# Kernel tuning notes

Hardware: AMD Instinct MI355X
Metric: run time of the kernel (lower is better)

## Reference

```python
import jax, jax.numpy as jnp
import numpy as np

B, N, M, DQ, DK, DV, H = 8, 1024, 1024, 512, 512, 512, 8
DH = DV // H           # per-head dim (dim_split)
DFF = 4 * DV           # FFN hidden dim
EPS = 1e-5


def _layernorm(x, g, b):
    mu = jnp.mean(x, axis=-1, keepdims=True)
    var = jnp.mean(jnp.square(x - mu), axis=-1, keepdims=True)
    return (x - mu) * jax.lax.rsqrt(var + EPS) * g + b


def setup_inputs() -> dict:
    key = jax.random.key(0)
    ks = jax.random.split(key, 20)
    s = 0.02
    return {
        "Q": jax.random.normal(ks[0], (B, N, DQ), jnp.float32),
        "K": jax.random.normal(ks[1], (B, M, DK), jnp.float32),
        "Wq": jax.random.normal(ks[2], (DV, DQ), jnp.float32) * s,
        "bq": jnp.zeros((DV,), jnp.float32),
        "Wk": jax.random.normal(ks[3], (DV, DK), jnp.float32) * s,
        "bk": jnp.zeros((DV,), jnp.float32),
        "Wv": jax.random.normal(ks[4], (DV, DK), jnp.float32) * s,
        "bv": jnp.zeros((DV,), jnp.float32),
        "W1": jax.random.normal(ks[5], (DFF, DV), jnp.float32) * s,
        "b1": jnp.zeros((DFF,), jnp.float32),
        "W2": jax.random.normal(ks[6], (DFF, DFF), jnp.float32) * s,
        "b2": jnp.zeros((DFF,), jnp.float32),
        "W3": jax.random.normal(ks[7], (DV, DFF), jnp.float32) * s,
        "b3": jnp.zeros((DV,), jnp.float32),
        "g0": jnp.ones((DV,), jnp.float32),
        "beta0": jnp.zeros((DV,), jnp.float32),
        "g1": jnp.ones((DV,), jnp.float32),
        "beta1": jnp.zeros((DV,), jnp.float32),
    }


def reference(Q, K, Wq, bq, Wk, bk, Wv, bv, W1, b1, W2, b2, W3, b3, g0, beta0, g1, beta1):
    # projections (torch Linear: x @ W.T + b)
    Qp = Q @ Wq.T + bq            # [B, N, DV]
    Kp = K @ Wk.T + bk            # [B, M, DV]
    Vp = K @ Wv.T + bv            # [B, M, DV]

    # split heads: [B, S, DV] -> [B, S, H, DH]
    Qh = Qp.reshape(B, N, H, DH)
    Kh = Kp.reshape(B, M, H, DH)
    Vh = Vp.reshape(B, M, H, DH)

    # scaled dot-product attention (scale = sqrt(head_dim))
    A = jnp.einsum("bnhd,bmhd->bhnm", Qh, Kh) / jnp.sqrt(jnp.float32(DH))
    A = jax.nn.softmax(A, axis=-1)
    O = jnp.einsum("bhnm,bmhd->bnhd", A, Vh).reshape(B, N, DV)

    # residual with projected Q, then LN
    O = _layernorm(O + Qp, g0, beta0)

    # FFN: Linear->ReLU->Linear->ReLU->Linear (num_hidden_layers=2)
    h = jax.nn.relu(O @ W1.T + b1)
    h = jax.nn.relu(h @ W2.T + b2)
    Off = h @ W3.T + b3

    return _layernorm(O + Off, g1, beta1)
```

## Files before the change

kernel.cpp:

```cpp
#include <hip/hip_runtime.h>


typedef __bf16 bf16_t;
typedef __bf16 bf16x8 __attribute__((ext_vector_type(8)));
typedef __bf16 bf16x4 __attribute__((ext_vector_type(4)));
typedef __bf16 bf16x2 __attribute__((ext_vector_type(2)));
typedef float  f32x4  __attribute__((ext_vector_type(4)));
typedef float  f32x16 __attribute__((ext_vector_type(16)));
typedef int    i32x4_t __attribute__((ext_vector_type(4)));
typedef int    i32x8_t __attribute__((ext_vector_type(8)));

__device__ __forceinline__ f32x4 mfma16(bf16x8 a, bf16x8 b, f32x4 c) {
  return __builtin_amdgcn_mfma_f32_16x16x32_bf16(a, b, c, 0, 0, 0);
}

__device__ __forceinline__ void gload_lds16(const void* g, void* l) {
  __builtin_amdgcn_global_load_lds((const __attribute__((address_space(1))) void*)g,
                                   (__attribute__((address_space(3))) void*)l,
                                   16, 0, 0);
}

__device__ __forceinline__ unsigned char to_fp8(float v) {
  return (unsigned char)(__builtin_amdgcn_cvt_pk_fp8_f32(v, v, 0, false) & 0xff);
}

__global__ __launch_bounds__(256) void cast_all(
    const float* __restrict__ Q, const float* __restrict__ K,
    const float* __restrict__ Wq, const float* __restrict__ Wk,
    const float* __restrict__ Wv, const float* __restrict__ W1,
    const float* __restrict__ W2, const float* __restrict__ W3,
    bf16_t* Qb, bf16_t* Kb, bf16_t* Wqb, bf16_t* Wkb, bf16_t* Wvb,
    bf16_t* W1b, unsigned char* W2q, bf16_t* W3b)
{
  long i = ((long)blockIdx.x * 256 + threadIdx.x) * 4;
  if (i >= 10223616L && i < 14417920L) {
    long o = i - 10223616L;
    float4 v = *(const float4*)(W2 + o);
    unsigned int lo = __builtin_amdgcn_cvt_pk_fp8_f32(v.x, v.y, 0, false);
    unsigned int hi = __builtin_amdgcn_cvt_pk_fp8_f32(v.z, v.w, 0, false);
    *(unsigned int*)(W2q + o) = (lo & 0xffffu) | (hi << 16);
    return;
  }
  const float* s; bf16_t* d; long o;
  if      (i <  4194304L) { s = Q;  d = Qb;  o = i;             }
  else if (i <  8388608L) { s = K;  d = Kb;  o = i - 4194304L;  }
  else if (i <  8650752L) { s = Wq; d = Wqb; o = i - 8388608L;  }
  else if (i <  8912896L) { s = Wk; d = Wkb; o = i - 8650752L;  }
  else if (i <  9175040L) { s = Wv; d = Wvb; o = i - 8912896L;  }
  else if (i < 10223616L) { s = W1; d = W1b; o = i - 9175040L;  }
  else                    { s = W3; d = W3b; o = i - 14417920L; }
  float4 v = *(const float4*)(s + o);
  bf16x4 w;
  w[0] = (bf16_t)v.x; w[1] = (bf16_t)v.y; w[2] = (bf16_t)v.z; w[3] = (bf16_t)v.w;
  *(bf16x4*)(d + o) = w;
}

template <int BM, bool RELU, bool VTEPI>
__device__ __forceinline__ void gemm_core(
    const bf16_t* __restrict__ A, const bf16_t* __restrict__ W,
    const float* __restrict__ bias, float* __restrict__ Cf,
    bf16_t* __restrict__ Cb, unsigned char* __restrict__ C8,
    bf16_t* __restrict__ VTout,
    float bscale, int N, int K, int lda, int ldb, int bx, int by)
{
  static_assert(BM == 128, "gemm_core tuned for BM=128");
  constexpr int FI = 4;
  constexpr int FJ = 4;
  constexpr int CN = 64;
  constexpr int AISS = 4;
  constexpr int SM_HALF = (BM + 128) * 64 * 2;
  constexpr int SMEM = 2 * SM_HALF;

  __shared__ __align__(16) char smem[SMEM];

  const int tid  = threadIdx.x;
  const int wave = tid >> 6, lane = tid & 63;
  const int lq   = lane & 15, quad = lane >> 4;
  const int wm   = wave & 1;
  const int wn   = wave >> 1;
  const long row0 = (long)bx * BM;
  const long col0 = (long)by * 128;

  const int sr = tid >> 3;
  const int cg = (tid & 7) ^ (sr & 7);
  const bf16_t* ag = A + (row0 + sr) * (long)lda + cg * 8;
  const bf16_t* bg = W + (col0 + sr) * (long)ldb + cg * 8;
  const int asOff = wave * 1024;
  const int bsOff = BM * 128 + wave * 1024;
  const long arows32 = 32L * lda;
  const long brows32 = 32L * ldb;

  auto stage = [&](int k0, int bi) {
    char* base = smem + bi * SM_HALF;
#pragma unroll
    for (int is = 0; is < AISS; is++)
      gload_lds16(ag + is * arows32 + k0, base + asOff + is * 4096);
#pragma unroll
    for (int is = 0; is < 4; is++)
      gload_lds16(bg + is * brows32 + k0, base + bsOff + is * 4096);
  };

  const int off0 = (quad ^ (lq & 7)) * 8;
  const int aO0 = ((wm * 64 + lq) * 64 + off0) * 2;
  const int aO1 = ((wm * 64 + lq) * 64 + (off0 ^ 32)) * 2;
  const int bO0 = BM * 128 + ((wn * CN + lq) * 64 + off0) * 2;
  const int bO1 = BM * 128 + ((wn * CN + lq) * 64 + (off0 ^ 32)) * 2;

  f32x4 acc[FI][FJ];
#pragma unroll
  for (int i = 0; i < FI; i++)
#pragma unroll
    for (int j = 0; j < FJ; j++) acc[i][j] = (f32x4){0.f, 0.f, 0.f, 0.f};

  stage(0, 0);
  const int nt = K >> 6;
  for (int t = 0; t < nt; ++t) {
    const int cur = t & 1;
    if (t < nt - 1) {
      stage((t + 1) * 64, cur ^ 1);
      asm volatile("s_waitcnt vmcnt(8)" ::: "memory");
    } else {
      asm volatile("s_waitcnt vmcnt(0)" ::: "memory");
    }
    __builtin_amdgcn_s_barrier();
    __builtin_amdgcn_sched_barrier(0);

    const char* base = smem + cur * SM_HALF;
    bf16x8 af[FI], bw[FJ];
#pragma unroll
    for (int i = 0; i < FI; i++) af[i] = *(const bf16x8*)(base + aO0 + i * 2048);
#pragma unroll
    for (int j = 0; j < FJ; j++) bw[j] = *(const bf16x8*)(base + bO0 + j * 2048);
#pragma unroll
    for (int i = 0; i < FI; i++)
#pragma unroll
      for (int j = 0; j < FJ; j++)
        acc[i][j] = mfma16(af[i], bw[j], acc[i][j]);
#pragma unroll
    for (int i = 0; i < FI; i++) af[i] = *(const bf16x8*)(base + aO1 + i * 2048);
#pragma unroll
    for (int j = 0; j < FJ; j++) bw[j] = *(const bf16x8*)(base + bO1 + j * 2048);
#pragma unroll
    for (int i = 0; i < FI; i++)
#pragma unroll
      for (int j = 0; j < FJ; j++)
        acc[i][j] = mfma16(af[i], bw[j], acc[i][j]);

    __builtin_amdgcn_sched_barrier(0);
    __builtin_amdgcn_s_barrier();
  }

  float bc[FJ];
#pragma unroll
  for (int j = 0; j < FJ; j++)
    bc[j] = bias ? bias[col0 + wn * CN + j * 16 + lq] : 0.f;

  if (VTEPI && VTout) {
    bf16_t* Ts = (bf16_t*)smem;
    __syncthreads();
#pragma unroll
    for (int i = 0; i < FI; i++)
#pragma unroll
      for (int j = 0; j < FJ; j++) {
        bf16x4 pv;
#pragma unroll
        for (int r = 0; r < 4; r++) pv[r] = (bf16_t)(acc[i][j][r] + bc[j]);
        *(bf16x4*)(Ts + (wn * CN + j * 16 + lq) * 132 + wm * 64 + i * 16 + quad * 4) = pv;
      }
    __syncthreads();
    const int b  = bx >> 3;
    const int mb = (bx & 7) * 128;
    const int h0 = by * 2;
    const int dd = tid >> 4;
    const int mc = (tid & 15) * 8;
#pragma unroll
    for (int p = 0; p < 8; p++) {
      const int d = dd + p * 16;
      bf16x8 v = *(const bf16x8*)(Ts + d * 132 + mc);
      *(bf16x8*)(VTout + ((long)(b * 8 + h0 + (d >> 6))) * 65536
                 + (d & 63) * 1024 + mb + mc) = v;
    }
    return;
  }

  const long rb = row0 + wm * 64 + quad * 4;
  const long cb = col0 + wn * CN + lq;
#pragma unroll
  for (int i = 0; i < FI; i++)
#pragma unroll
    for (int j = 0; j < FJ; j++)
#pragma unroll
      for (int r = 0; r < 4; r++) {
        float v = acc[i][j][r] + bc[j];
        if (RELU) v = fmaxf(v, 0.f);
        long idx = (rb + i * 16 + r) * (long)N + cb + j * 16;
        if (Cf) Cf[idx] = v;
        if (Cb) Cb[idx] = (bf16_t)(v * bscale);
        if (C8) C8[idx] = to_fp8(v);
      }
}

template <int BM, bool RELU>
__global__ __launch_bounds__(256) void gemm_bt(
    const bf16_t* __restrict__ A, const bf16_t* __restrict__ W,
    const float* __restrict__ bias, float* __restrict__ Cf,
    bf16_t* __restrict__ Cb, unsigned char* __restrict__ C8,
    float bscale, int N, int K)
{
  const int d  = blockIdx.x;
  const int bx = (d & 7) * 8 + ((d >> 3) & 7);
  const int by = d >> 6;
  gemm_core<BM, RELU, false>(A, W, bias, Cf, Cb, C8, nullptr, bscale,
                             N, K, K, K, bx, by);
}

__global__ __launch_bounds__(256) void ffn3_splitk(
    const bf16_t* __restrict__ H2, const bf16_t* __restrict__ W3b,
    bf16_t* __restrict__ Off01)
{
  const int z = blockIdx.z;
  gemm_core<128, false, false>(H2 + z * 1024, W3b + z * 1024, nullptr,
                               nullptr, Off01 + (long)z * 4194304, nullptr,
                               nullptr, 1.0f, 512, 1024, 2048, 2048,
                               blockIdx.x, blockIdx.y);
}

__global__ __launch_bounds__(256) void proj3(
    const bf16_t* __restrict__ Qb, const bf16_t* __restrict__ Kb,
    const bf16_t* __restrict__ Wqb, const bf16_t* __restrict__ Wkb,
    const bf16_t* __restrict__ Wvb,
    const float* __restrict__ bq, const float* __restrict__ bk,
    const float* __restrict__ bv,
    bf16_t* Qpb, bf16_t* Kpb, bf16_t* VT)
{
  const int z = blockIdx.z;
  const bf16_t* A  = (z == 0) ? Qb : Kb;
  const bf16_t* Wt = (z == 0) ? Wqb : ((z == 1) ? Wkb : Wvb);
  const float* bias = (z == 0) ? bq : ((z == 1) ? bk : bv);
  bf16_t* Cb = (z == 0) ? Qpb : ((z == 1) ? Kpb : nullptr);
  bf16_t* VTout = (z == 2) ? VT : nullptr;
  const float sc = (z == 1) ? 0.125f : 1.0f;
  gemm_core<128, false, true>(A, Wt, bias, nullptr, Cb, nullptr, VTout, sc,
                              512, 512, 512, 512, blockIdx.x, blockIdx.y);
}

__global__ __launch_bounds__(256) void ffn2_fp8(
    const unsigned char* __restrict__ H1, const unsigned char* __restrict__ W2,
    const float* __restrict__ bias, bf16_t* __restrict__ C)
{
  __shared__ unsigned char As[2][16384];
  __shared__ unsigned char Bs[2][16384];
  const int tid = threadIdx.x;
  const int wave = tid >> 6, lane = tid & 63;
  const int wm = wave & 1, wn = wave >> 1;
  const int m = lane & 31, h = lane >> 5;
  const int d  = blockIdx.x;
  const int bxi = (d & 7) * 8 + ((d >> 3) & 7);
  const int byi = d >> 6;
  const long row0 = (long)bxi * 128;
  const long col0 = (long)byi * 128;

  const int sr = tid >> 3;
  const int cg = (tid & 7) ^ (sr & 7);
  const unsigned char* ag = H1 + (row0 + sr) * 2048 + cg * 16;
  const unsigned char* bg = W2 + (col0 + sr) * 2048 + cg * 16;

  auto stage = [&](int k0, int bi) {
    char* asD = (char*)As[bi] + wave * 1024;
    char* bsD = (char*)Bs[bi] + wave * 1024;
#pragma unroll
    for (int is = 0; is < 4; is++)
      gload_lds16(ag + is * 65536 + k0, asD + is * 4096);
#pragma unroll
    for (int is = 0; is < 4; is++)
      gload_lds16(bg + is * 65536 + k0, bsD + is * 4096);
  };

  const int ar0 = wm * 64 + m, ar1 = ar0 + 32;
  const int br0 = wn * 64 + m, br1 = wn * 64 + 32 + m;

  f32x16 acc[2][2];
#pragma unroll
  for (int mi = 0; mi < 2; mi++)
#pragma unroll
    for (int nj = 0; nj < 2; nj++)
#pragma unroll
      for (int r = 0; r < 16; r++) acc[mi][nj][r] = 0.f;

  stage(0, 0);
  for (int t = 0; t < 16; ++t) {
    const int cur = t & 1;
    if (t < 15) {
      stage((t + 1) * 128, cur ^ 1);
      asm volatile("s_waitcnt vmcnt(8)" ::: "memory");
    } else {
      asm volatile("s_waitcnt vmcnt(0)" ::: "memory");
    }
    __builtin_amdgcn_s_barrier();
    __builtin_amdgcn_sched_barrier(0);

    const unsigned char* Ac = As[cur];
    const unsigned char* Bc = Bs[cur];
#pragma unroll
    for (int ks = 0; ks < 2; ks++) {
      const int c0 = ks * 4 + h * 2;
      i32x8_t a[2], b[2];
#pragma unroll
      for (int mi = 0; mi < 2; mi++) {
        const int r = mi ? ar1 : ar0;
        i32x4_t lo = *(const i32x4_t*)(Ac + r * 128 + ((c0    ) ^ (r & 7)) * 16);
        i32x4_t hi = *(const i32x4_t*)(Ac + r * 128 + ((c0 + 1) ^ (r & 7)) * 16);
        a[mi][0] = lo[0]; a[mi][1] = lo[1]; a[mi][2] = lo[2]; a[mi][3] = lo[3];
        a[mi][4] = hi[0]; a[mi][5] = hi[1]; a[mi][6] = hi[2]; a[mi][7] = hi[3];
      }
#pragma unroll
      for (int nj = 0; nj < 2; nj++) {
        const int r = nj ? br1 : br0;
        i32x4_t lo = *(const i32x4_t*)(Bc + r * 128 + ((c0    ) ^ (r & 7)) * 16);
        i32x4_t hi = *(const i32x4_t*)(Bc + r * 128 + ((c0 + 1) ^ (r & 7)) * 16);
        b[nj][0] = lo[0]; b[nj][1] = lo[1]; b[nj][2] = lo[2]; b[nj][3] = lo[3];
        b[nj][4] = hi[0]; b[nj][5] = hi[1]; b[nj][6] = hi[2]; b[nj][7] = hi[3];
      }
#pragma unroll
      for (int mi = 0; mi < 2; mi++)
#pragma unroll
        for (int nj = 0; nj < 2; nj++)
          acc[mi][nj] = __builtin_amdgcn_mfma_scale_f32_32x32x64_f8f6f4(
              a[mi], b[nj], acc[mi][nj], 0, 0,
              0, 0x7f7f7f7f, 0, 0x7f7f7f7f);
    }

    __builtin_amdgcn_sched_barrier(0);
    __builtin_amdgcn_s_barrier();
  }

  float bc[2];
  bc[0] = bias[col0 + wn * 64 + m];
  bc[1] = bias[col0 + wn * 64 + 32 + m];
#pragma unroll
  for (int mi = 0; mi < 2; mi++)
#pragma unroll
    for (int nj = 0; nj < 2; nj++)
#pragma unroll
      for (int reg = 0; reg < 16; reg++) {
        const int rl = (reg & 3) + 8 * (reg >> 2) + 4 * h;
        float v = fmaxf(acc[mi][nj][reg] + bc[nj], 0.f);
        C[(row0 + wm * 64 + mi * 32 + rl) * 2048 + col0 + wn * 64 + nj * 32 + m]
            = (bf16_t)v;
      }
}

__global__ __launch_bounds__(256) void attn(
    const bf16_t* __restrict__ Qp, const bf16_t* __restrict__ Kp,
    const bf16_t* __restrict__ VT, bf16_t* __restrict__ O)
{
  const int d0 = blockIdx.x;
  const int j  = d0 >> 3;
  const int g  = (d0 & 7) * 8 + (j >> 3);
  const int qb = j & 7;
  const int h  = g & 7, b = g >> 3;

  const int tid = threadIdx.x;
  const int wave = tid >> 6, lane = tid & 63;
  const int lq = lane & 15, quad = lane >> 4;

  __shared__ bf16_t Ks[2][8192];
  __shared__ bf16_t VTs[2][8192];
  __shared__ bf16_t Ps[4][16 * 72];

  const long bh = (long)b * 1024;
  const int qrowA = qb * 128 + wave * 16 + lq;
  const int qrowB = qrowA + 64;

  const bf16_t* qpA = Qp + (bh + qrowA) * 512 + h * 64 + quad * 8;
  const bf16_t* qpB = Qp + (bh + qrowB) * 512 + h * 64 + quad * 8;
  const bf16x8 qfA0 = *(const bf16x8*)qpA;
  const bf16x8 qfA1 = *(const bf16x8*)(qpA + 32);
  const bf16x8 qfB0 = *(const bf16x8*)qpB;
  const bf16x8 qfB1 = *(const bf16x8*)(qpB + 32);

  f32x4 oaccA[4], oaccB[4];
#pragma unroll
  for (int t = 0; t < 4; t++) {
    oaccA[t] = (f32x4){0.f, 0.f, 0.f, 0.f};
    oaccB[t] = (f32x4){0.f, 0.f, 0.f, 0.f};
  }
  float lA = 0.f, lB = 0.f;

  const int sr = tid >> 3;
  const int cg = (tid & 7) ^ (sr & 7);
  const bf16_t* kg  = Kp + bh * 512 + h * 64;
  const bf16_t* vtg = VT + ((long)b * 8 + h) * 65536;
  const int off0 = (quad ^ (lq & 7)) * 8;

  auto stage = [&](int m0, int bi) {
    char* ksDst = (char*)(Ks[bi]) + wave * 1024;
    char* vtDst = (char*)(VTs[bi]) + wave * 1024;
#pragma unroll
    for (int s = 0; s < 2; s++) {
      gload_lds16(kg + (long)(m0 + s * 64 + sr) * 512 + cg * 8,      ksDst + s * 8192);
      gload_lds16(kg + (long)(m0 + s * 64 + sr + 32) * 512 + cg * 8, ksDst + s * 8192 + 4096);
      gload_lds16(vtg + (long)sr * 1024 + m0 + s * 64 + cg * 8,        vtDst + s * 8192);
      gload_lds16(vtg + (long)(sr + 32) * 1024 + m0 + s * 64 + cg * 8, vtDst + s * 8192 + 4096);
    }
  };

  stage(0, 0);

  for (int t = 0; t < 8; ++t) {
    const int cur = t & 1;
    if (t < 7) {
      stage((t + 1) * 128, cur ^ 1);
      asm volatile("s_waitcnt vmcnt(8)" ::: "memory");
    } else {
      asm volatile("s_waitcnt vmcnt(0)" ::: "memory");
    }
    __builtin_amdgcn_s_barrier();
    __builtin_amdgcn_sched_barrier(0);

    const bf16_t* Kc = Ks[cur];
    const bf16_t* Vc = VTs[cur];

    f32x4 stA[8], stB[8];
#pragma unroll
    for (int tt = 0; tt < 8; tt++) {
      const bf16_t* kb = Kc + (tt >> 2) * 4096 + ((tt & 3) * 16 + lq) * 64;
      bf16x8 ka0 = *(const bf16x8*)(kb + off0);
      bf16x8 ka1 = *(const bf16x8*)(kb + (off0 ^ 32));
      f32x4 sA = (f32x4){0.f, 0.f, 0.f, 0.f};
      sA = mfma16(ka0, qfA0, sA);
      sA = mfma16(ka1, qfA1, sA);
      stA[tt] = sA;
      f32x4 sB = (f32x4){0.f, 0.f, 0.f, 0.f};
      sB = mfma16(ka0, qfB0, sB);
      sB = mfma16(ka1, qfB1, sB);
      stB[tt] = sB;
    }

    float lsA = 0.f, lsB = 0.f;
#pragma unroll
    for (int tt = 0; tt < 8; tt++)
#pragma unroll
      for (int r = 0; r < 4; r++) {
        float pA = __expf(stA[tt][r]);
        stA[tt][r] = pA;
        lsA += pA;
        float pB = __expf(stB[tt][r]);
        stB[tt][r] = pB;
        lsB += pB;
      }
    lsA += __shfl_xor(lsA, 16, 64);
    lsA += __shfl_xor(lsA, 32, 64);
    lA += lsA;
    lsB += __shfl_xor(lsB, 16, 64);
    lsB += __shfl_xor(lsB, 32, 64);
    lB += lsB;

    bf16_t* pw = &Ps[wave][0];
#pragma unroll
    for (int hh = 0; hh < 2; hh++) {
#pragma unroll
      for (int tt = 0; tt < 4; tt++) {
        bf16x4 pv;
#pragma unroll
        for (int r = 0; r < 4; r++) pv[r] = (bf16_t)stA[hh * 4 + tt][r];
        *(bf16x4*)(pw + lq * 72 + tt * 16 + quad * 4) = pv;
      }
#pragma unroll
      for (int ks = 0; ks < 2; ks++) {
        bf16x8 pb = *(const bf16x8*)(pw + lq * 72 + ks * 32 + quad * 8);
#pragma unroll
        for (int dt = 0; dt < 4; dt++) {
          const bf16_t* vb = Vc + hh * 4096 + (dt * 16 + lq) * 64;
          bf16x8 va = *(const bf16x8*)(vb + (ks ? (off0 ^ 32) : off0));
          oaccA[dt] = mfma16(va, pb, oaccA[dt]);
        }
      }
    }
#pragma unroll
    for (int hh = 0; hh < 2; hh++) {
#pragma unroll
      for (int tt = 0; tt < 4; tt++) {
        bf16x4 pv;
#pragma unroll
        for (int r = 0; r < 4; r++) pv[r] = (bf16_t)stB[hh * 4 + tt][r];
        *(bf16x4*)(pw + lq * 72 + tt * 16 + quad * 4) = pv;
      }
#pragma unroll
      for (int ks = 0; ks < 2; ks++) {
        bf16x8 pb = *(const bf16x8*)(pw + lq * 72 + ks * 32 + quad * 8);
#pragma unroll
        for (int dt = 0; dt < 4; dt++) {
          const bf16_t* vb = Vc + hh * 4096 + (dt * 16 + lq) * 64;
          bf16x8 va = *(const bf16x8*)(vb + (ks ? (off0 ^ 32) : off0));
          oaccB[dt] = mfma16(va, pb, oaccB[dt]);
        }
      }
    }

    __builtin_amdgcn_sched_barrier(0);
    __builtin_amdgcn_s_barrier();
  }

  const float invA = 1.f / lA;
  const float invB = 1.f / lB;
  bf16_t* opA = O + (bh + qrowA) * 512 + h * 64 + quad * 4;
  bf16_t* opB = O + (bh + qrowB) * 512 + h * 64 + quad * 4;
#pragma unroll
  for (int dt = 0; dt < 4; dt++) {
    bf16x4 vA, vB;
#pragma unroll
    for (int r = 0; r < 4; r++) {
      vA[r] = (bf16_t)(oaccA[dt][r] * invA);
      vB[r] = (bf16_t)(oaccB[dt][r] * invB);
    }
    *(bf16x4*)(opA + dt * 16) = vA;
    *(bf16x4*)(opB + dt * 16) = vB;
  }
}

__device__ __forceinline__ float2 ld2(const float* p, long row, int tid) {
  return ((const float2*)(p + row * 512))[tid];
}
__device__ __forceinline__ float2 ld2(const bf16_t* p, long row, int tid) {
  bf16x2 v = *(const bf16x2*)(p + row * 512 + tid * 2);
  return make_float2((float)v[0], (float)v[1]);
}

__device__ __forceinline__ void ln_finish(
    float x0, float x1, const float* g, const float* be, int tid,
    int wave, int lane, float* of, bf16_t* ob, long row)
{
  float s = x0 + x1, ss = x0 * x0 + x1 * x1;
#pragma unroll
  for (int off = 1; off < 64; off <<= 1) {
    s  += __shfl_xor(s,  off, 64);
    ss += __shfl_xor(ss, off, 64);
  }
  __shared__ float sm[8];
  if (lane == 0) { sm[wave] = s; sm[4 + wave] = ss; }
  __syncthreads();
  s  = sm[0] + sm[1] + sm[2] + sm[3];
  ss = sm[4] + sm[5] + sm[6] + sm[7];
  const float mu = s * (1.f / 512.f);
  const float var = ss * (1.f / 512.f) - mu * mu;
  const float rs = rsqrtf(var + 1e-5f);
  const float2 gg = ((const float2*)g)[tid];
  const float2 bb = ((const float2*)be)[tid];
  const float o0 = (x0 - mu) * rs * gg.x + bb.x;
  const float o1 = (x1 - mu) * rs * gg.y + bb.y;
  if (of) ((float2*)(of + row * 512))[tid] = make_float2(o0, o1);
  if (ob) {
    bf16x2 t; t[0] = (bf16_t)o0; t[1] = (bf16_t)o1;
    *(bf16x2*)(ob + row * 512 + tid * 2) = t;
  }
}

__global__ __launch_bounds__(256) void ln_res(
    const bf16_t* __restrict__ A, const bf16_t* __restrict__ Bv,
    const float* __restrict__ g, const float* __restrict__ be,
    bf16_t* __restrict__ ob)
{
  const int row = blockIdx.x, tid = threadIdx.x;
  const float2 va = ld2(A,  (long)row, tid);
  const float2 vb = ld2(Bv, (long)row, tid);
  ln_finish(va.x + vb.x, va.y + vb.y, g, be, tid, tid >> 6, tid & 63,
            nullptr, ob, row);
}

__global__ __launch_bounds__(256) void ln_res3(
    const bf16_t* __restrict__ X, const bf16_t* __restrict__ O0,
    const bf16_t* __restrict__ O1, const float* __restrict__ bias,
    const float* __restrict__ g, const float* __restrict__ be,
    float* __restrict__ of)
{
  const int row = blockIdx.x, tid = threadIdx.x;
  const float2 vx = ld2(X,  (long)row, tid);
  const float2 v0 = ld2(O0, (long)row, tid);
  const float2 v1 = ld2(O1, (long)row, tid);
  const float2 vb = ((const float2*)bias)[tid];
  ln_finish(vx.x + v0.x + v1.x + vb.x, vx.y + v0.y + v1.y + vb.y,
            g, be, tid, tid >> 6, tid & 63, of, nullptr, row);
}

extern "C" void kernel_launch(void* const* d_in, const int* in_sizes, int n_in,
                              void* d_out, int out_size, void* d_ws, size_t ws_size,
                              hipStream_t stream)
{
  const float* Q   = (const float*)d_in[0];
  const float* K   = (const float*)d_in[1];
  const float* Wq  = (const float*)d_in[2];
  const float* bq  = (const float*)d_in[3];
  const float* Wk  = (const float*)d_in[4];
  const float* bk  = (const float*)d_in[5];
  const float* Wv  = (const float*)d_in[6];
  const float* bv  = (const float*)d_in[7];
  const float* W1  = (const float*)d_in[8];
  const float* b1  = (const float*)d_in[9];
  const float* W2  = (const float*)d_in[10];
  const float* b2  = (const float*)d_in[11];
  const float* W3  = (const float*)d_in[12];
  const float* b3  = (const float*)d_in[13];
  const float* g0  = (const float*)d_in[14];
  const float* be0 = (const float*)d_in[15];
  const float* g1  = (const float*)d_in[16];
  const float* be1 = (const float*)d_in[17];

  char* ws = (char*)d_ws;
  bf16_t* Wqb = (bf16_t*)(ws + 0);
  bf16_t* Wkb = (bf16_t*)(ws + 524288);
  bf16_t* Wvb = (bf16_t*)(ws + 1048576);
  bf16_t* W1b = (bf16_t*)(ws + 1572864);
  bf16_t* W3b = (bf16_t*)(ws + 3670016);
  unsigned char* W2q = (unsigned char*)(ws + 5767168);
  bf16_t* Qb  = (bf16_t*)(ws + 14155776);
  bf16_t* Kb  = (bf16_t*)(ws + 22544384);
  bf16_t* Qpb = (bf16_t*)(ws + 30932992);
  bf16_t* Kpb = (bf16_t*)(ws + 39321600);
  bf16_t* VT  = (bf16_t*)(ws + 47710208);
  bf16_t* Of  = (bf16_t*)(ws + 14155776);
  bf16_t* Xb  = (bf16_t*)(ws + 22544384);
  bf16_t* H2  = (bf16_t*)(ws + 30932992);
  unsigned char* H1q = (unsigned char*)(ws + 64487424);
  bf16_t* Off0 = (bf16_t*)(ws + 64487424);
  bf16_t* Off1 = (bf16_t*)(ws + 72876032);
  float*  out = (float*)d_out;

  cast_all<<<15104, 256, 0, stream>>>(Q, K, Wq, Wk, Wv, W1, W2, W3,
                                      Qb, Kb, Wqb, Wkb, Wvb, W1b, W2q, W3b);
  proj3<<<dim3(64, 4, 3), 256, 0, stream>>>(Qb, Kb, Wqb, Wkb, Wvb, bq, bk, bv,
                                            Qpb, Kpb, VT);
  attn<<<dim3(512, 1, 1), 256, 0, stream>>>(Qpb, Kpb, VT, Of);
  ln_res<<<8192, 256, 0, stream>>>(Of, Qpb, g0, be0, Xb);
  gemm_bt<128, true ><<<dim3(1024, 1, 1), 256, 0, stream>>>(Xb, W1b, b1, nullptr, nullptr, H1q, 1.0f, 2048, 512);
  ffn2_fp8<<<dim3(1024, 1, 1), 256, 0, stream>>>(H1q, W2q, b2, H2);
  ffn3_splitk<<<dim3(64, 4, 2), 256, 0, stream>>>(H2, W3b, Off0);
  ln_res3<<<8192, 256, 0, stream>>>(Xb, Off0, Off1, b3, g1, be1, out);
}
```

Before: 271.4 us.

## Drop double buffering in ffn2, ffn3 and projection GEMMs to halve LDS

Adds a DBUF template flag to the shared GEMM core. The projection and FFN3 split-K kernels now use one LDS buffer with a sync, load, sync sequence per K tile, and the FP8 FFN2 kernel gets the same single-buffer loop. Halving shared memory per block should let more blocks fit on each CU, hiding latency through occupancy rather than in-block prefetch. The cost is that loads no longer overlap MFMA work inside a block, and each tile needs two full barriers.

```diff
diff --git a/kernel.cpp b/kernel.cpp
--- a/kernel.cpp
+++ b/kernel.cpp
@@ -55,7 +55,7 @@
   *(bf16x4*)(d + o) = w;
 }
 
-template <int BM, bool RELU, bool VTEPI>
+template <int BM, bool RELU, bool VTEPI, bool DBUF>
 __device__ __forceinline__ void gemm_core(
     const bf16_t* __restrict__ A, const bf16_t* __restrict__ W,
     const float* __restrict__ bias, float* __restrict__ Cf,
@@ -68,8 +68,10 @@
   constexpr int FJ = 4;
   constexpr int CN = 64;
   constexpr int AISS = 4;
-  constexpr int SM_HALF = (BM + 128) * 64 * 2;
-  constexpr int SMEM = 2 * SM_HALF;
+  constexpr int SM_AB = (BM + 128) * 64 * 2;
+  constexpr int SM_TS = 128 * 132 * 2;
+  constexpr int SM_ONE = (VTEPI && SM_TS > SM_AB) ? SM_TS : SM_AB;
+  constexpr int SMEM = DBUF ? 2 * SM_AB : SM_ONE;
 
   __shared__ __align__(16) char smem[SMEM];
 
@@ -91,7 +93,7 @@
   const long brows32 = 32L * ldb;
 
   auto stage = [&](int k0, int bi) {
-    char* base = smem + bi * SM_HALF;
+    char* base = smem + (DBUF ? bi * SM_AB : 0);
 #pragma unroll
     for (int is = 0; is < AISS; is++)
       gload_lds16(ag + is * arows32 + k0, base + asOff + is * 4096);
@@ -112,20 +114,28 @@
 #pragma unroll
     for (int j = 0; j < FJ; j++) acc[i][j] = (f32x4){0.f, 0.f, 0.f, 0.f};
 
-  stage(0, 0);
   const int nt = K >> 6;
+  if constexpr (DBUF) stage(0, 0);
   for (int t = 0; t < nt; ++t) {
-    const int cur = t & 1;
-    if (t < nt - 1) {
-      stage((t + 1) * 64, cur ^ 1);
-      asm volatile("s_waitcnt vmcnt(8)" ::: "memory");
+    const char* base;
+    if constexpr (DBUF) {
+      const int cur = t & 1;
+      if (t < nt - 1) {
+        stage((t + 1) * 64, cur ^ 1);
+        asm volatile("s_waitcnt vmcnt(8)" ::: "memory");
+      } else {
+        asm volatile("s_waitcnt vmcnt(0)" ::: "memory");
+      }
+      __builtin_amdgcn_s_barrier();
+      __builtin_amdgcn_sched_barrier(0);
+      base = smem + cur * SM_AB;
     } else {
-      asm volatile("s_waitcnt vmcnt(0)" ::: "memory");
-    }
-    __builtin_amdgcn_s_barrier();
-    __builtin_amdgcn_sched_barrier(0);
-
-    const char* base = smem + cur * SM_HALF;
+      __syncthreads();
+      stage(t * 64, 0);
+      __syncthreads();
+      base = smem;
+    }
+
     bf16x8 af[FI], bw[FJ];
 #pragma unroll
     for (int i = 0; i < FI; i++) af[i] = *(const bf16x8*)(base + aO0 + i * 2048);
@@ -146,8 +156,10 @@
       for (int j = 0; j < FJ; j++)
         acc[i][j] = mfma16(af[i], bw[j], acc[i][j]);
 
-    __builtin_amdgcn_sched_barrier(0);
-    __builtin_amdgcn_s_barrier();
+    if constexpr (DBUF) {
+      __builtin_amdgcn_sched_barrier(0);
+      __builtin_amdgcn_s_barrier();
+    }
   }
 
   float bc[FJ];
@@ -210,8 +222,8 @@
   const int d  = blockIdx.x;
   const int bx = (d & 7) * 8 + ((d >> 3) & 7);
   const int by = d >> 6;
-  gemm_core<BM, RELU, false>(A, W, bias, Cf, Cb, C8, nullptr, bscale,
-                             N, K, K, K, bx, by);
+  gemm_core<BM, RELU, false, true>(A, W, bias, Cf, Cb, C8, nullptr, bscale,
+                                   N, K, K, K, bx, by);
 }
 
 __global__ __launch_bounds__(256) void ffn3_splitk(
@@ -219,7 +231,7 @@
     bf16_t* __restrict__ Off01)
 {
   const int z = blockIdx.z;
-  gemm_core<128, false, false>(H2 + z * 1024, W3b + z * 1024, nullptr,
+  gemm_core<128, false, false, false>(H2 + z * 1024, W3b + z * 1024, nullptr,
                                nullptr, Off01 + (long)z * 4194304, nullptr,
                                nullptr, 1.0f, 512, 1024, 2048, 2048,
                                blockIdx.x, blockIdx.y);
@@ -240,7 +252,7 @@
   bf16_t* Cb = (z == 0) ? Qpb : ((z == 1) ? Kpb : nullptr);
   bf16_t* VTout = (z == 2) ? VT : nullptr;
   const float sc = (z == 1) ? 0.125f : 1.0f;
-  gemm_core<128, false, true>(A, Wt, bias, nullptr, Cb, nullptr, VTout, sc,
+  gemm_core<128, false, true, false>(A, Wt, bias, nullptr, Cb, nullptr, VTout, sc,
                               512, 512, 512, 512, blockIdx.x, blockIdx.y);
 }
 
@@ -248,8 +260,8 @@
     const unsigned char* __restrict__ H1, const unsigned char* __restrict__ W2,
     const float* __restrict__ bias, bf16_t* __restrict__ C)
 {
-  __shared__ unsigned char As[2][16384];
-  __shared__ unsigned char Bs[2][16384];
+  __shared__ unsigned char As[16384];
+  __shared__ unsigned char Bs[16384];
   const int tid = threadIdx.x;
   const int wave = tid >> 6, lane = tid & 63;
   const int wm = wave & 1, wn = wave >> 1;
@@ -264,43 +276,29 @@
   const int cg = (tid & 7) ^ (sr & 7);
   const unsigned char* ag = H1 + (row0 + sr) * 2048 + cg * 16;
   const unsigned char* bg = W2 + (col0 + sr) * 2048 + cg * 16;
-
-  auto stage = [&](int k0, int bi) {
-    char* asD = (char*)As[bi] + wave * 1024;
-    char* bsD = (char*)Bs[bi] + wave * 1024;
+  char* asD = (char*)As + wave * 1024;
+  char* bsD = (char*)Bs + wave * 1024;
+
+  const int ar0 = wm * 64 + m, ar1 = ar0 + 32;
+  const int br0 = wn * 64 + m, br1 = wn * 64 + 32 + m;
+
+  f32x16 acc[2][2];
+#pragma unroll
+  for (int mi = 0; mi < 2; mi++)
+#pragma unroll
+    for (int nj = 0; nj < 2; nj++)
+#pragma unroll
+      for (int r = 0; r < 16; r++) acc[mi][nj][r] = 0.f;
+
+  for (int k0 = 0; k0 < 2048; k0 += 128) {
+    __syncthreads();
 #pragma unroll
     for (int is = 0; is < 4; is++)
       gload_lds16(ag + is * 65536 + k0, asD + is * 4096);
 #pragma unroll
     for (int is = 0; is < 4; is++)
       gload_lds16(bg + is * 65536 + k0, bsD + is * 4096);
-  };
-
-  const int ar0 = wm * 64 + m, ar1 = ar0 + 32;
-  const int br0 = wn * 64 + m, br1 = wn * 64 + 32 + m;
-
-  f32x16 acc[2][2];
-#pragma unroll
-  for (int mi = 0; mi < 2; mi++)
-#pragma unroll
-    for (int nj = 0; nj < 2; nj++)
-#pragma unroll
-      for (int r = 0; r < 16; r++) acc[mi][nj][r] = 0.f;
-
-  stage(0, 0);
-  for (int t = 0; t < 16; ++t) {
-    const int cur = t & 1;
-    if (t < 15) {
-      stage((t + 1) * 128, cur ^ 1);
-      asm volatile("s_waitcnt vmcnt(8)" ::: "memory");
-    } else {
-      asm volatile("s_waitcnt vmcnt(0)" ::: "memory");
-    }
-    __builtin_amdgcn_s_barrier();
-    __builtin_amdgcn_sched_barrier(0);
-
-    const unsigned char* Ac = As[cur];
-    const unsigned char* Bc = Bs[cur];
+    __syncthreads();
 #pragma unroll
     for (int ks = 0; ks < 2; ks++) {
       const int c0 = ks * 4 + h * 2;
@@ -308,16 +306,16 @@
 #pragma unroll
       for (int mi = 0; mi < 2; mi++) {
         const int r = mi ? ar1 : ar0;
-        i32x4_t lo = *(const i32x4_t*)(Ac + r * 128 + ((c0    ) ^ (r & 7)) * 16);
-        i32x4_t hi = *(const i32x4_t*)(Ac + r * 128 + ((c0 + 1) ^ (r & 7)) * 16);
+        i32x4_t lo = *(const i32x4_t*)(As + r * 128 + ((c0    ) ^ (r & 7)) * 16);
+        i32x4_t hi = *(const i32x4_t*)(As + r * 128 + ((c0 + 1) ^ (r & 7)) * 16);
         a[mi][0] = lo[0]; a[mi][1] = lo[1]; a[mi][2] = lo[2]; a[mi][3] = lo[3];
         a[mi][4] = hi[0]; a[mi][5] = hi[1]; a[mi][6] = hi[2]; a[mi][7] = hi[3];
       }
 #pragma unroll
       for (int nj = 0; nj < 2; nj++) {
         const int r = nj ? br1 : br0;
-        i32x4_t lo = *(const i32x4_t*)(Bc + r * 128 + ((c0    ) ^ (r & 7)) * 16);
-        i32x4_t hi = *(const i32x4_t*)(Bc + r * 128 + ((c0 + 1) ^ (r & 7)) * 16);
+        i32x4_t lo = *(const i32x4_t*)(Bs + r * 128 + ((c0    ) ^ (r & 7)) * 16);
+        i32x4_t hi = *(const i32x4_t*)(Bs + r * 128 + ((c0 + 1) ^ (r & 7)) * 16);
         b[nj][0] = lo[0]; b[nj][1] = lo[1]; b[nj][2] = lo[2]; b[nj][3] = lo[3];
         b[nj][4] = hi[0]; b[nj][5] = hi[1]; b[nj][6] = hi[2]; b[nj][7] = hi[3];
       }
@@ -329,9 +327,6 @@
               a[mi], b[nj], acc[mi][nj], 0, 0,
               0, 0x7f7f7f7f, 0, 0x7f7f7f7f);
     }
-
-    __builtin_amdgcn_sched_barrier(0);
-    __builtin_amdgcn_s_barrier();
   }
 
   float bc[2];
```

Measured after the change: 274.6 us. About the same (+1.2%).
